# Kernel optimization log

Measured on AMD Instinct MI355X. Metric: run time of the kernel, lower is better.

The kernel has to match this reference:

```python
import jax, jax.numpy as jnp
import numpy as np

N = 262144
LOC_ENC_LEN = 60
NUM_WEIGHTS = 8
INDIM = 32
OUTDIM = 32
HIDDEN = 32
NEG_SLOPE = 0.01  # nn.LeakyReLU default


def _linear_init(key, fan_in, fan_out):
    # torch nn.Linear default: U(-1/sqrt(fan_in), 1/sqrt(fan_in))
    kw, kb = jax.random.split(key)
    bound = 1.0 / np.sqrt(fan_in)
    w = jax.random.uniform(kw, (fan_in, fan_out), jnp.float32, -bound, bound)
    b = jax.random.uniform(kb, (fan_out,), jnp.float32, -bound, bound)
    return w, b


def setup_inputs() -> dict:
    key = jax.random.key(0)
    ks = jax.random.split(key, 10)
    rel_loc_feat = jax.random.normal(ks[0], (N, LOC_ENC_LEN), jnp.float32)
    feat = jax.random.normal(ks[1], (N, INDIM), jnp.float32)
    dims = [LOC_ENC_LEN, HIDDEN, HIDDEN, HIDDEN, HIDDEN, HIDDEN, NUM_WEIGHTS]
    params = {}
    for i in range(6):
        w, b = _linear_init(ks[2 + i], dims[i], dims[i + 1])
        params[f'sn_w{i}'] = w
        params[f'sn_b{i}'] = b
    # weights_bank: kaiming_normal on [num_weights, indim*outdim] -> std = sqrt(2/fan_in), fan_in = indim*outdim
    std = np.sqrt(2.0 / (INDIM * OUTDIM))
    params['bank'] = jax.random.normal(ks[9], (NUM_WEIGHTS, INDIM * OUTDIM), jnp.float32) * std
    return {'rel_loc_feat': rel_loc_feat, 'feat': feat, **params}


def _score_net(x, ws, bs):
    # 5 Linear+LeakyReLU blocks, then final Linear (no activation)
    for i in range(5):
        x = x @ ws[i] + bs[i]
        x = jnp.where(x >= 0, x, NEG_SLOPE * x)
    return x @ ws[5] + bs[5]


def reference(rel_loc_feat, feat,
              sn_w0, sn_b0, sn_w1, sn_b1, sn_w2, sn_b2,
              sn_w3, sn_b3, sn_w4, sn_b4, sn_w5, sn_b5, bank):
    ws = [sn_w0, sn_w1, sn_w2, sn_w3, sn_w4, sn_w5]
    bs = [sn_b0, sn_b1, sn_b2, sn_b3, sn_b4, sn_b5]
    logits = _score_net(rel_loc_feat, ws, bs)          # [N, num_weights]
    coeff = jax.nn.softmax(logits, axis=-1)            # [N, num_weights]
    # per-point weight matrix: [N, indim*outdim] -> [N, indim, outdim]
    weights = (coeff @ bank).reshape(coeff.shape[0], INDIM, OUTDIM)
    # per-point matmul: feat[:, None] @ weights -> squeeze
    out = jnp.einsum('ni,nio->no', feat, weights)      # [N, outdim]
    return out
```

## Files before the change

kernel.cpp:

```cpp
#include <hip/hip_runtime.h>
#include <stdint.h>


typedef __attribute__((ext_vector_type(8))) __bf16 bf16x8;
typedef __attribute__((ext_vector_type(2))) __bf16 bf16x2;
typedef __attribute__((ext_vector_type(4))) float f32x4;

union FragU { uint32_t u[4]; bf16x8 v; uint4 q; };

__device__ __forceinline__ unsigned short f2bf(float f) {
    union { float f; uint32_t i; } v; v.f = f;
    return (unsigned short)((v.i + 0x7FFFu + ((v.i >> 16) & 1u)) >> 16);
}
__device__ __forceinline__ float bf2f(uint32_t u16) {
    union { uint32_t i; float f; } v; v.i = u16 << 16; return v.f;
}
__device__ __forceinline__ uint32_t pk2(float x, float y) {
    union { bf16x2 h; uint32_t u; } c;
    c.h[0] = (__bf16)x; c.h[1] = (__bf16)y;
    return c.u;
}
__device__ __forceinline__ bf16x8 pack8(float a, float b, float c, float d,
                                        float e, float f, float g, float h) {
    bf16x8 v;
    v[0] = (__bf16)a; v[1] = (__bf16)b; v[2] = (__bf16)c; v[3] = (__bf16)d;
    v[4] = (__bf16)e; v[5] = (__bf16)f; v[6] = (__bf16)g; v[7] = (__bf16)h;
    return v;
}
__device__ __forceinline__ int permK(int k) {
    return 4 * (k >> 3) + (k & 3) + 16 * ((k >> 2) & 1);
}
__device__ __forceinline__ f32x4 MF(bf16x8 a, bf16x8 b, f32x4 c) {
    return __builtin_amdgcn_mfma_f32_16x16x32_bf16(a, b, c, 0, 0, 0);
}


struct WPf { const float* p[13]; };

__global__ void pc_prep(WPf wp, uint32_t* __restrict__ ws) {
    int idx = blockIdx.x * blockDim.x + threadIdx.x;
    if (idx >= 10240) return;
    if (idx < 7424) {
        int layer, t, chunk = 0, lane, d; const float* w; bool perm;
        int r = idx;
        if (r < 1024) { chunk = r >> 9; r &= 511; t = r >> 8; r &= 255; lane = r >> 2; d = r & 3;
                        layer = 0; w = wp.p[0]; perm = false; }
        else if (r < 3072) { r -= 1024; layer = 1 + (r >> 9); r &= 511; t = r >> 8; r &= 255;
                             lane = r >> 2; d = r & 3; w = wp.p[2 * layer]; perm = true; }
        else if (r < 3328) { r -= 3072; layer = 5; t = 0; lane = r >> 2; d = r & 3;
                             w = wp.p[10]; perm = true; }
        else { r -= 3328; int bk = r >> 9; r &= 511; t = r >> 8; r &= 255; lane = r >> 2; d = r & 3;
               layer = -1; w = wp.p[12] + bk * 1024; perm = false; }
        int gq = lane >> 4, m = t * 16 + (lane & 15);
        uint32_t o = 0;
        #pragma unroll
        for (int e = 0; e < 2; ++e) {
            int kf = 8 * gq + 2 * d + e;
            float v = 0.f;
            if (layer == -1) {
                v = w[kf * 32 + m];
            } else {
                int ks = perm ? permK(kf) : (chunk * 32 + kf);
                if (layer == 0)      { if (ks < 60) v = w[ks * 32 + m]; }
                else if (layer == 5) { if (m < 8)   v = w[ks * 8 + m]; }
                else                 v = w[ks * 32 + m];
            }
            o |= ((uint32_t)f2bf(v)) << (16 * e);
        }
        ws[idx] = o;
    } else if (idx < 9984) {
        int r = idx - 7424; int L = r >> 9; r &= 511; int t = r >> 8; r &= 255;
        int lane = r >> 2, rr = r & 3;
        ((float*)ws)[idx] = wp.p[2 * L + 1][t * 16 + 4 * (lane >> 4) + rr];
    } else {
        int r = idx - 9984; int lane = r >> 2, rr = r & 3;
        int m = 4 * (lane >> 4) + rr;
        ((float*)ws)[idx] = (m < 8) ? wp.p[11][m] : 0.f;
    }
}


#define CO 10240

__global__ __launch_bounds__(256, 3) void pc_main(
    const float* __restrict__ rel, const float* __restrict__ feat,
    const uint32_t* __restrict__ wsu, float* __restrict__ out)
{
    __shared__ __align__(16) uint32_t W[10752];

    const int lane = threadIdx.x & 63;
    const int wv = threadIdx.x >> 6;
    const int g = lane >> 4;
    const int n16 = lane & 15;
    const size_t nA = (size_t)blockIdx.x * 128 + wv * 32 + n16;

    float4 ra[2], rb[2], rc[2], rd[2], fa[2], fb[2];
    #pragma unroll
    for (int q = 0; q < 2; ++q) {
        const float* rrow = rel + (nA + 16 * q) * 60;
        ra[q] = *(const float4*)(rrow + 8 * g);
        rb[q] = *(const float4*)(rrow + 8 * g + 4);
        rc[q] = *(const float4*)(rrow + 32 + 8 * g);
        rd[q] = make_float4(0.f, 0.f, 0.f, 0.f);
        if (g < 3) rd[q] = *(const float4*)(rrow + 36 + 8 * g);
        const float* frow = feat + (nA + 16 * q) * 32 + 8 * g;
        fa[q] = *(const float4*)frow;
        fb[q] = *(const float4*)(frow + 4);
    }

    {
        uint4* s4 = (uint4*)W;
        const uint4* g4 = (const uint4*)wsu;
        #pragma unroll
        for (int i = 0; i < 10; ++i) {
            int idx = threadIdx.x + 256 * i;
            int src = (idx < 832) ? idx
                    : (idx < 1536) ? idx + 1024
                    : idx - 704;
            s4[idx] = g4[src];
        }
    }
    __syncthreads();

    #define LDF(off) ({ FragU _f; _f.q = ((const uint4*)(W + (off)))[lane]; _f.v; })
    #define LDB(off) ({ float4 _b = ((const float4*)(W + (off)))[lane]; \
                        (f32x4){_b.x, _b.y, _b.z, _b.w}; })

    {
        bf16x8 c0[2], c1[2];
        #pragma unroll
        for (int q = 0; q < 2; ++q) {
            c0[q] = pack8(ra[q].x, ra[q].y, ra[q].z, ra[q].w,
                          rb[q].x, rb[q].y, rb[q].z, rb[q].w);
            c1[q] = pack8(rc[q].x, rc[q].y, rc[q].z, rc[q].w,
                          rd[q].x, rd[q].y, rd[q].z, rd[q].w);
        }

        f32x4 t0[2], t1[2];
        {
            f32x4 ba = LDB(3328), bb = LDB(3328 + 256);
            bf16x8 w00 = LDF(0), w01 = LDF(256), w10 = LDF(512), w11 = LDF(768);
            #pragma unroll
            for (int q = 0; q < 2; ++q) {
                t0[q] = MF(w00, c0[q], ba);    t1[q] = MF(w01, c0[q], bb);
                t0[q] = MF(w10, c1[q], t0[q]); t1[q] = MF(w11, c1[q], t1[q]);
            }
        }

        #pragma unroll
        for (int L = 0; L < 4; ++L) {
            bf16x8 wa = LDF(1024 + L * 512), wb = LDF(1024 + L * 512 + 256);
            f32x4 ba = LDB(3328 + (L + 1) * 512), bb = LDB(3328 + (L + 1) * 512 + 256);
            #pragma unroll
            for (int q = 0; q < 2; ++q) {
                #pragma unroll
                for (int r = 0; r < 4; ++r) {
                    t0[q][r] = fmaxf(t0[q][r], 0.01f * t0[q][r]);
                    t1[q][r] = fmaxf(t1[q][r], 0.01f * t1[q][r]);
                }
                bf16x8 bx = pack8(t0[q][0], t0[q][1], t0[q][2], t0[q][3],
                                  t1[q][0], t1[q][1], t1[q][2], t1[q][3]);
                t0[q] = MF(wa, bx, ba);
                t1[q] = MF(wb, bx, bb);
            }
        }

        {
            bf16x8 w5 = LDF(3072);
            f32x4 b5 = LDB(5888);
            #pragma unroll
            for (int q = 0; q < 2; ++q) {
                #pragma unroll
                for (int r = 0; r < 4; ++r) {
                    t0[q][r] = fmaxf(t0[q][r], 0.01f * t0[q][r]);
                    t1[q][r] = fmaxf(t1[q][r], 0.01f * t1[q][r]);
                }
                bf16x8 bx = pack8(t0[q][0], t0[q][1], t0[q][2], t0[q][3],
                                  t1[q][0], t1[q][1], t1[q][2], t1[q][3]);
                t0[q] = MF(w5, bx, b5);
            }
        }

        #pragma unroll
        for (int q = 0; q < 2; ++q) {
            float m4 = fmaxf(fmaxf(t0[q][0], t0[q][1]), fmaxf(t0[q][2], t0[q][3]));
            float m8 = fmaxf(m4, __shfl_xor(m4, 16, 64));
            float e0 = __expf(t0[q][0] - m8), e1 = __expf(t0[q][1] - m8);
            float e2 = __expf(t0[q][2] - m8), e3 = __expf(t0[q][3] - m8);
            float s4 = e0 + e1 + e2 + e3;
            float s8 = s4 + __shfl_xor(s4, 16, 64);
            float inv = 1.0f / s8;
            uint32_t p01 = pk2(e0 * inv, e1 * inv);
            uint32_t p23 = pk2(e2 * inv, e3 * inv);
            if (g < 2) {
                int p = wv * 32 + q * 16 + n16;
                *(uint2*)(W + CO + p * 4 + 2 * g) = make_uint2(p01, p23);
            }
        }
    }

    {
        uint4 cp[2];
        #pragma unroll
        for (int q = 0; q < 2; ++q)
            cp[q] = *(const uint4*)(W + CO + (wv * 32 + q * 16 + n16) * 4);

        bf16x8 bfr[2];
        #pragma unroll
        for (int q = 0; q < 2; ++q)
            bfr[q] = pack8(fa[q].x, fa[q].y, fa[q].z, fa[q].w,
                           fb[q].x, fb[q].y, fb[q].z, fb[q].w);

        float cw[2][8];
        #pragma unroll
        for (int q = 0; q < 2; ++q) {
            cw[q][0] = bf2f(cp[q].x & 0xffff); cw[q][1] = bf2f(cp[q].x >> 16);
            cw[q][2] = bf2f(cp[q].y & 0xffff); cw[q][3] = bf2f(cp[q].y >> 16);
            cw[q][4] = bf2f(cp[q].z & 0xffff); cw[q][5] = bf2f(cp[q].z >> 16);
            cw[q][6] = bf2f(cp[q].w & 0xffff); cw[q][7] = bf2f(cp[q].w >> 16);
        }

        f32x4 o0[2], o1[2];
        #pragma unroll
        for (int q = 0; q < 2; ++q) {
            o0[q] = (f32x4){0.f, 0.f, 0.f, 0.f};
            o1[q] = (f32x4){0.f, 0.f, 0.f, 0.f};
        }
        #pragma unroll
        for (int k = 0; k < 8; ++k) {
            bf16x8 wk0 = LDF(6144 + k * 512), wk1 = LDF(6144 + k * 512 + 256);
            #pragma unroll
            for (int q = 0; q < 2; ++q) {
                f32x4 z = {0.f, 0.f, 0.f, 0.f};
                f32x4 u0 = MF(wk0, bfr[q], z);
                f32x4 u1 = MF(wk1, bfr[q], z);
                #pragma unroll
                for (int r = 0; r < 4; ++r) {
                    o0[q][r] += cw[q][k] * u0[r];
                    o1[q][r] += cw[q][k] * u1[r];
                }
            }
        }

        #pragma unroll
        for (int q = 0; q < 2; ++q) {
            float* orow = out + (nA + 16 * q) * 32;
            *(float4*)(orow + 4 * g)      = make_float4(o0[q][0], o0[q][1], o0[q][2], o0[q][3]);
            *(float4*)(orow + 16 + 4 * g) = make_float4(o1[q][0], o1[q][1], o1[q][2], o1[q][3]);
        }
    }
    #undef LDF
    #undef LDB
}

extern "C" void kernel_launch(void* const* d_in, const int* in_sizes, int n_in,
                              void* d_out, int out_size, void* d_ws, size_t ws_size,
                              hipStream_t stream)
{
    const float* rel = (const float*)d_in[0];
    const float* feat = (const float*)d_in[1];
    WPf wp;
    for (int i = 0; i < 13; ++i) wp.p[i] = (const float*)d_in[2 + i];
    uint32_t* ws = (uint32_t*)d_ws;
    float* out = (float*)d_out;

    const int npts = in_sizes[0] / 60;
    const int nblocks = npts / 128;

    hipLaunchKernelGGL(pc_prep, dim3(40), dim3(256), 0, stream, wp, ws);
    hipLaunchKernelGGL(pc_main, dim3(nblocks), dim3(256), 0, stream, rel, feat, ws, out);
}
```

Measured before the change: 160.5 us.

## Compact bias layout in shared memory and process two tiles per block

Biases are now stored compactly (32 floats per layer) instead of replicated per-lane fragments, which shrinks the shared-memory weight staging and the per-block global-to-LDS copy. Each block now loops over two 128-point tiles, so the weight staging and the barrier are paid once per 256 points. The grid is halved. In exchange, each block does twice the serial work, and the next tile's loads are not prefetched across iterations.

```diff
diff --git a/kernel.cpp b/kernel.cpp
--- a/kernel.cpp
+++ b/kernel.cpp
@@ -39,7 +39,7 @@
 
 __global__ void pc_prep(WPf wp, uint32_t* __restrict__ ws) {
     int idx = blockIdx.x * blockDim.x + threadIdx.x;
-    if (idx >= 10240) return;
+    if (idx >= 7616) return;
     if (idx < 7424) {
         int layer, t, chunk = 0, lane, d; const float* w; bool perm;
         int r = idx;
@@ -68,185 +68,184 @@
             o |= ((uint32_t)f2bf(v)) << (16 * e);
         }
         ws[idx] = o;
-    } else if (idx < 9984) {
-        int r = idx - 7424; int L = r >> 9; r &= 511; int t = r >> 8; r &= 255;
-        int lane = r >> 2, rr = r & 3;
-        ((float*)ws)[idx] = wp.p[2 * L + 1][t * 16 + 4 * (lane >> 4) + rr];
     } else {
-        int r = idx - 9984; int lane = r >> 2, rr = r & 3;
-        int m = 4 * (lane >> 4) + rr;
-        ((float*)ws)[idx] = (m < 8) ? wp.p[11][m] : 0.f;
+        int r = idx - 7424; int L = r >> 5, m = r & 31;
+        float v;
+        if (L < 5)      v = wp.p[2 * L + 1][m];
+        else            v = (m < 8) ? wp.p[11][m] : 0.f;
+        ((float*)ws)[idx] = v;
     }
 }
 
-
-#define CO 10240
+#define IT 2
+
+#define CO 7616
 
 __global__ __launch_bounds__(256, 3) void pc_main(
     const float* __restrict__ rel, const float* __restrict__ feat,
     const uint32_t* __restrict__ wsu, float* __restrict__ out)
 {
-    __shared__ __align__(16) uint32_t W[10752];
+    __shared__ __align__(16) uint32_t W[8640];
+    {
+        uint4* s4 = (uint4*)W;
+        const uint4* g4 = (const uint4*)wsu;
+        #pragma unroll
+        for (int i = 0; i < 8; ++i) {
+            int idx = threadIdx.x + 256 * i;
+            if (idx < 1904) s4[idx] = g4[idx];
+        }
+    }
+    __syncthreads();
 
     const int lane = threadIdx.x & 63;
     const int wv = threadIdx.x >> 6;
     const int g = lane >> 4;
     const int n16 = lane & 15;
-    const size_t nA = (size_t)blockIdx.x * 128 + wv * 32 + n16;
-
-    float4 ra[2], rb[2], rc[2], rd[2], fa[2], fb[2];
+    const size_t pt0 = (size_t)blockIdx.x * 256 + wv * 64;
+
+    #define LDF(off) ({ FragU _f; _f.q = ((const uint4*)(W + (off)))[lane]; _f.v; })
+    #define LDB(L, t) ({ float4 _b = *(const float4*)((const float*)(W + 7424) + (L) * 32 + (t) * 16 + 4 * g); \
+                         (f32x4){_b.x, _b.y, _b.z, _b.w}; })
+
     #pragma unroll
-    for (int q = 0; q < 2; ++q) {
-        const float* rrow = rel + (nA + 16 * q) * 60;
-        ra[q] = *(const float4*)(rrow + 8 * g);
-        rb[q] = *(const float4*)(rrow + 8 * g + 4);
-        rc[q] = *(const float4*)(rrow + 32 + 8 * g);
-        rd[q] = make_float4(0.f, 0.f, 0.f, 0.f);
-        if (g < 3) rd[q] = *(const float4*)(rrow + 36 + 8 * g);
-        const float* frow = feat + (nA + 16 * q) * 32 + 8 * g;
-        fa[q] = *(const float4*)frow;
-        fb[q] = *(const float4*)(frow + 4);
-    }
-
-    {
-        uint4* s4 = (uint4*)W;
-        const uint4* g4 = (const uint4*)wsu;
-        #pragma unroll
-        for (int i = 0; i < 10; ++i) {
-            int idx = threadIdx.x + 256 * i;
-            int src = (idx < 832) ? idx
-                    : (idx < 1536) ? idx + 1024
-                    : idx - 704;
-            s4[idx] = g4[src];
-        }
-    }
-    __syncthreads();
-
-    #define LDF(off) ({ FragU _f; _f.q = ((const uint4*)(W + (off)))[lane]; _f.v; })
-    #define LDB(off) ({ float4 _b = ((const float4*)(W + (off)))[lane]; \
-                        (f32x4){_b.x, _b.y, _b.z, _b.w}; })
-
-    {
-        bf16x8 c0[2], c1[2];
+    for (int it = 0; it < IT; ++it) {
+        const size_t nA = pt0 + it * 32 + n16;
+        const int cbase = CO + it * 512 + wv * 128;
+
+        float4 ra[2], rb[2], rc[2], rd[2], fa[2], fb[2];
         #pragma unroll
         for (int q = 0; q < 2; ++q) {
-            c0[q] = pack8(ra[q].x, ra[q].y, ra[q].z, ra[q].w,
-                          rb[q].x, rb[q].y, rb[q].z, rb[q].w);
-            c1[q] = pack8(rc[q].x, rc[q].y, rc[q].z, rc[q].w,
-                          rd[q].x, rd[q].y, rd[q].z, rd[q].w);
-        }
-
-        f32x4 t0[2], t1[2];
+            const float* rrow = rel + (nA + 16 * q) * 60;
+            ra[q] = *(const float4*)(rrow + 8 * g);
+            rb[q] = *(const float4*)(rrow + 8 * g + 4);
+            rc[q] = *(const float4*)(rrow + 32 + 8 * g);
+            rd[q] = make_float4(0.f, 0.f, 0.f, 0.f);
+            if (g < 3) rd[q] = *(const float4*)(rrow + 36 + 8 * g);
+            const float* frow = feat + (nA + 16 * q) * 32 + 8 * g;
+            fa[q] = *(const float4*)frow;
+            fb[q] = *(const float4*)(frow + 4);
+        }
+
         {
-            f32x4 ba = LDB(3328), bb = LDB(3328 + 256);
-            bf16x8 w00 = LDF(0), w01 = LDF(256), w10 = LDF(512), w11 = LDF(768);
-            #pragma unroll
-            for (int q = 0; q < 2; ++q) {
-                t0[q] = MF(w00, c0[q], ba);    t1[q] = MF(w01, c0[q], bb);
-                t0[q] = MF(w10, c1[q], t0[q]); t1[q] = MF(w11, c1[q], t1[q]);
-            }
-        }
-
-        #pragma unroll
-        for (int L = 0; L < 4; ++L) {
-            bf16x8 wa = LDF(1024 + L * 512), wb = LDF(1024 + L * 512 + 256);
-            f32x4 ba = LDB(3328 + (L + 1) * 512), bb = LDB(3328 + (L + 1) * 512 + 256);
-            #pragma unroll
-            for (int q = 0; q < 2; ++q) {
-                #pragma unroll
-                for (int r = 0; r < 4; ++r) {
-                    t0[q][r] = fmaxf(t0[q][r], 0.01f * t0[q][r]);
-                    t1[q][r] = fmaxf(t1[q][r], 0.01f * t1[q][r]);
-                }
-                bf16x8 bx = pack8(t0[q][0], t0[q][1], t0[q][2], t0[q][3],
-                                  t1[q][0], t1[q][1], t1[q][2], t1[q][3]);
-                t0[q] = MF(wa, bx, ba);
-                t1[q] = MF(wb, bx, bb);
+            bf16x8 c0[2], c1[2];
+            #pragma unroll
+            for (int q = 0; q < 2; ++q) {
+                c0[q] = pack8(ra[q].x, ra[q].y, ra[q].z, ra[q].w,
+                              rb[q].x, rb[q].y, rb[q].z, rb[q].w);
+                c1[q] = pack8(rc[q].x, rc[q].y, rc[q].z, rc[q].w,
+                              rd[q].x, rd[q].y, rd[q].z, rd[q].w);
+            }
+
+            f32x4 t0[2], t1[2];
+            {
+                f32x4 ba = LDB(0, 0), bb = LDB(0, 1);
+                bf16x8 w00 = LDF(0), w01 = LDF(256), w10 = LDF(512), w11 = LDF(768);
+                #pragma unroll
+                for (int q = 0; q < 2; ++q) {
+                    t0[q] = MF(w00, c0[q], ba);    t1[q] = MF(w01, c0[q], bb);
+                    t0[q] = MF(w10, c1[q], t0[q]); t1[q] = MF(w11, c1[q], t1[q]);
+                }
+            }
+
+            #pragma unroll
+            for (int L = 0; L < 4; ++L) {
+                bf16x8 wa = LDF(1024 + L * 512), wb = LDF(1024 + L * 512 + 256);
+                f32x4 ba = LDB(L + 1, 0), bb = LDB(L + 1, 1);
+                #pragma unroll
+                for (int q = 0; q < 2; ++q) {
+                    #pragma unroll
+                    for (int r = 0; r < 4; ++r) {
+                        t0[q][r] = fmaxf(t0[q][r], 0.01f * t0[q][r]);
+                        t1[q][r] = fmaxf(t1[q][r], 0.01f * t1[q][r]);
+                    }
+                    bf16x8 bx = pack8(t0[q][0], t0[q][1], t0[q][2], t0[q][3],
+                                      t1[q][0], t1[q][1], t1[q][2], t1[q][3]);
+                    t0[q] = MF(wa, bx, ba);
+                    t1[q] = MF(wb, bx, bb);
+                }
+            }
+
+            {
+                bf16x8 w5 = LDF(3072);
+                f32x4 b5 = LDB(5, 0);
+                #pragma unroll
+                for (int q = 0; q < 2; ++q) {
+                    #pragma unroll
+                    for (int r = 0; r < 4; ++r) {
+                        t0[q][r] = fmaxf(t0[q][r], 0.01f * t0[q][r]);
+                        t1[q][r] = fmaxf(t1[q][r], 0.01f * t1[q][r]);
+                    }
+                    bf16x8 bx = pack8(t0[q][0], t0[q][1], t0[q][2], t0[q][3],
+                                      t1[q][0], t1[q][1], t1[q][2], t1[q][3]);
+                    t0[q] = MF(w5, bx, b5);
+                }
+            }
+
+            #pragma unroll
+            for (int q = 0; q < 2; ++q) {
+                float m4 = fmaxf(fmaxf(t0[q][0], t0[q][1]), fmaxf(t0[q][2], t0[q][3]));
+                float m8 = fmaxf(m4, __shfl_xor(m4, 16, 64));
+                float e0 = __expf(t0[q][0] - m8), e1 = __expf(t0[q][1] - m8);
+                float e2 = __expf(t0[q][2] - m8), e3 = __expf(t0[q][3] - m8);
+                float s4 = e0 + e1 + e2 + e3;
+                float s8 = s4 + __shfl_xor(s4, 16, 64);
+                float inv = 1.0f / s8;
+                uint32_t p01 = pk2(e0 * inv, e1 * inv);
+                uint32_t p23 = pk2(e2 * inv, e3 * inv);
+                if (g < 2)
+                    *(uint2*)(W + cbase + (q * 16 + n16) * 4 + 2 * g) = make_uint2(p01, p23);
             }
         }
 
         {
-            bf16x8 w5 = LDF(3072);
-            f32x4 b5 = LDB(5888);
-            #pragma unroll
-            for (int q = 0; q < 2; ++q) {
-                #pragma unroll
-                for (int r = 0; r < 4; ++r) {
-                    t0[q][r] = fmaxf(t0[q][r], 0.01f * t0[q][r]);
-                    t1[q][r] = fmaxf(t1[q][r], 0.01f * t1[q][r]);
-                }
-                bf16x8 bx = pack8(t0[q][0], t0[q][1], t0[q][2], t0[q][3],
-                                  t1[q][0], t1[q][1], t1[q][2], t1[q][3]);
-                t0[q] = MF(w5, bx, b5);
-            }
-        }
-
-        #pragma unroll
-        for (int q = 0; q < 2; ++q) {
-            float m4 = fmaxf(fmaxf(t0[q][0], t0[q][1]), fmaxf(t0[q][2], t0[q][3]));
-            float m8 = fmaxf(m4, __shfl_xor(m4, 16, 64));
-            float e0 = __expf(t0[q][0] - m8), e1 = __expf(t0[q][1] - m8);
-            float e2 = __expf(t0[q][2] - m8), e3 = __expf(t0[q][3] - m8);
-            float s4 = e0 + e1 + e2 + e3;
-            float s8 = s4 + __shfl_xor(s4, 16, 64);
-            float inv = 1.0f / s8;
-            uint32_t p01 = pk2(e0 * inv, e1 * inv);
-            uint32_t p23 = pk2(e2 * inv, e3 * inv);
-            if (g < 2) {
-                int p = wv * 32 + q * 16 + n16;
-                *(uint2*)(W + CO + p * 4 + 2 * g) = make_uint2(p01, p23);
-            }
-        }
-    }
-
-    {
-        uint4 cp[2];
-        #pragma unroll
-        for (int q = 0; q < 2; ++q)
-            cp[q] = *(const uint4*)(W + CO + (wv * 32 + q * 16 + n16) * 4);
-
-        bf16x8 bfr[2];
-        #pragma unroll
-        for (int q = 0; q < 2; ++q)
-            bfr[q] = pack8(fa[q].x, fa[q].y, fa[q].z, fa[q].w,
-                           fb[q].x, fb[q].y, fb[q].z, fb[q].w);
-
-        float cw[2][8];
-        #pragma unroll
-        for (int q = 0; q < 2; ++q) {
-            cw[q][0] = bf2f(cp[q].x & 0xffff); cw[q][1] = bf2f(cp[q].x >> 16);
-            cw[q][2] = bf2f(cp[q].y & 0xffff); cw[q][3] = bf2f(cp[q].y >> 16);
-            cw[q][4] = bf2f(cp[q].z & 0xffff); cw[q][5] = bf2f(cp[q].z >> 16);
-            cw[q][6] = bf2f(cp[q].w & 0xffff); cw[q][7] = bf2f(cp[q].w >> 16);
-        }
-
-        f32x4 o0[2], o1[2];
-        #pragma unroll
-        for (int q = 0; q < 2; ++q) {
-            o0[q] = (f32x4){0.f, 0.f, 0.f, 0.f};
-            o1[q] = (f32x4){0.f, 0.f, 0.f, 0.f};
-        }
-        #pragma unroll
-        for (int k = 0; k < 8; ++k) {
-            bf16x8 wk0 = LDF(6144 + k * 512), wk1 = LDF(6144 + k * 512 + 256);
-            #pragma unroll
-            for (int q = 0; q < 2; ++q) {
-                f32x4 z = {0.f, 0.f, 0.f, 0.f};
-                f32x4 u0 = MF(wk0, bfr[q], z);
-                f32x4 u1 = MF(wk1, bfr[q], z);
-                #pragma unroll
-                for (int r = 0; r < 4; ++r) {
-                    o0[q][r] += cw[q][k] * u0[r];
-                    o1[q][r] += cw[q][k] * u1[r];
-                }
-            }
-        }
-
-        #pragma unroll
-        for (int q = 0; q < 2; ++q) {
-            float* orow = out + (nA + 16 * q) * 32;
-            *(float4*)(orow + 4 * g)      = make_float4(o0[q][0], o0[q][1], o0[q][2], o0[q][3]);
-            *(float4*)(orow + 16 + 4 * g) = make_float4(o1[q][0], o1[q][1], o1[q][2], o1[q][3]);
+            uint4 cp[2];
+            #pragma unroll
+            for (int q = 0; q < 2; ++q)
+                cp[q] = *(const uint4*)(W + cbase + (q * 16 + n16) * 4);
+
+            bf16x8 bfr[2];
+            #pragma unroll
+            for (int q = 0; q < 2; ++q)
+                bfr[q] = pack8(fa[q].x, fa[q].y, fa[q].z, fa[q].w,
+                               fb[q].x, fb[q].y, fb[q].z, fb[q].w);
+
+            float cw[2][8];
+            #pragma unroll
+            for (int q = 0; q < 2; ++q) {
+                cw[q][0] = bf2f(cp[q].x & 0xffff); cw[q][1] = bf2f(cp[q].x >> 16);
+                cw[q][2] = bf2f(cp[q].y & 0xffff); cw[q][3] = bf2f(cp[q].y >> 16);
+                cw[q][4] = bf2f(cp[q].z & 0xffff); cw[q][5] = bf2f(cp[q].z >> 16);
+                cw[q][6] = bf2f(cp[q].w & 0xffff); cw[q][7] = bf2f(cp[q].w >> 16);
+            }
+
+            f32x4 o0[2], o1[2];
+            #pragma unroll
+            for (int q = 0; q < 2; ++q) {
+                o0[q] = (f32x4){0.f, 0.f, 0.f, 0.f};
+                o1[q] = (f32x4){0.f, 0.f, 0.f, 0.f};
+            }
+            #pragma unroll
+            for (int k = 0; k < 8; ++k) {
+                bf16x8 wk0 = LDF(3328 + k * 512), wk1 = LDF(3328 + k * 512 + 256);
+                #pragma unroll
+                for (int q = 0; q < 2; ++q) {
+                    f32x4 z = {0.f, 0.f, 0.f, 0.f};
+                    f32x4 u0 = MF(wk0, bfr[q], z);
+                    f32x4 u1 = MF(wk1, bfr[q], z);
+                    #pragma unroll
+                    for (int r = 0; r < 4; ++r) {
+                        o0[q][r] += cw[q][k] * u0[r];
+                        o1[q][r] += cw[q][k] * u1[r];
+                    }
+                }
+            }
+
+            #pragma unroll
+            for (int q = 0; q < 2; ++q) {
+                float* orow = out + (nA + 16 * q) * 32;
+                *(float4*)(orow + 4 * g)      = make_float4(o0[q][0], o0[q][1], o0[q][2], o0[q][3]);
+                *(float4*)(orow + 16 + 4 * g) = make_float4(o1[q][0], o1[q][1], o1[q][2], o1[q][3]);
+            }
         }
     }
     #undef LDF
@@ -265,8 +264,8 @@
     float* out = (float*)d_out;
 
     const int npts = in_sizes[0] / 60;
-    const int nblocks = npts / 128;
-
-    hipLaunchKernelGGL(pc_prep, dim3(40), dim3(256), 0, stream, wp, ws);
+    const int nblocks = npts / 256;
+
+    hipLaunchKernelGGL(pc_prep, dim3(30), dim3(256), 0, stream, wp, ws);
     hipLaunchKernelGGL(pc_main, dim3(nblocks), dim3(256), 0, stream, rel, feat, ws, out);
 }
```

New measurement: 161.8 us. Within noise of the previous version (+0.8%).
